# Performance work log

Measured on AMD Instinct MI355X. Metric: run time of the kernel, lower is better.

Reference implementation:

```python
import jax, jax.numpy as jnp
import numpy as np

NUM_HEADS = 8
NUM_GROUPS = 32
EPS = 1e-5


def group_norm(x, gamma, beta):
    # x: (B, C, N)
    B, C, N = x.shape
    xg = x.reshape(B, NUM_GROUPS, (C // NUM_GROUPS) * N)
    mean = xg.mean(axis=-1, keepdims=True)
    var = xg.var(axis=-1, keepdims=True)
    xg = (xg - mean) * jax.lax.rsqrt(var + EPS)
    x = xg.reshape(B, C, N)
    return x * gamma[None, :, None] + beta[None, :, None]


def setup_inputs() -> dict:
    key = jax.random.key(0)
    ks = jax.random.split(key, 7)
    B, C, H, W = 16, 512, 32, 32
    return {
        "x": jax.random.normal(ks[0], (B, C, H, W), dtype=jnp.float32),
        "gamma": jax.random.uniform(ks[1], (C,), dtype=jnp.float32, minval=0.5, maxval=1.5),
        "beta": jax.random.normal(ks[2], (C,), dtype=jnp.float32) * 0.1,
        "w_qkv": jax.random.normal(ks[3], (3 * C, C), dtype=jnp.float32) * 0.02,
        "b_qkv": jax.random.normal(ks[4], (3 * C,), dtype=jnp.float32) * 0.01,
        "w_proj": jax.random.normal(ks[5], (C, C), dtype=jnp.float32) * 0.02,
        "b_proj": jax.random.normal(ks[6], (C,), dtype=jnp.float32) * 0.01,
    }


def reference(x, gamma, beta, w_qkv, b_qkv, w_proj, b_proj):
    B, C, Hs, Ws = x.shape
    N = Hs * Ws
    x3 = x.reshape(B, C, N)
    xn = group_norm(x3, gamma, beta)
    # 1x1 Conv1d == channel-wise linear: (3C, C) x (B, C, N) -> (B, 3C, N)
    qkv = jnp.einsum('oc,bcn->bon', w_qkv, xn) + b_qkv[None, :, None]
    ch = C // NUM_HEADS
    qkv = qkv.reshape(B * NUM_HEADS, 3 * ch, N)
    q, k, v = jnp.split(qkv, 3, axis=1)  # each (B*H, ch, N)
    scale = ch ** (-0.25)
    w = jnp.einsum('bct,bcs->bts', q * scale, k * scale)  # (B*H, N, N)
    w = jax.nn.softmax(w.astype(jnp.float32), axis=-1).astype(q.dtype)
    h = jnp.einsum('bts,bcs->bct', w, v)  # (B*H, ch, N)
    h = h.reshape(B, C, N)
    h = jnp.einsum('oc,bcn->bon', w_proj, h) + b_proj[None, :, None]
    return (x3 + h).reshape(B, C, Hs, Ws)
```

## Files before the change

### kernel.cpp

```cpp
#include <hip/hip_runtime.h>
#include <stdint.h>

typedef unsigned short u16;
typedef float f32x4 __attribute__((ext_vector_type(4)));
typedef short bf16x8 __attribute__((ext_vector_type(8)));

#define DEV __device__ __forceinline__

DEV u16 f2bf(float f) {
  union { float f; unsigned int u; } v; v.f = f;
  unsigned int u = v.u;
  u = (u + 0x7FFFu + ((u >> 16) & 1u)) >> 16;
  return (u16)u;
}

DEV float exp2_(float x) {
#if __has_builtin(__builtin_amdgcn_exp2f)
  return __builtin_amdgcn_exp2f(x);
#else
  return exp2f(x);
#endif
}

DEV unsigned int cvt_pk_bf16(float lo, float hi) {
  unsigned int r;
  asm("v_cvt_pk_bf16_f32 %0, %1, %2" : "=v"(r) : "v"(lo), "v"(hi));
  return r;
}

typedef __attribute__((address_space(1))) const unsigned int* gas_t;
typedef __attribute__((address_space(3))) unsigned int* las_t;
DEV void gload16(const void* g, void* l) {
  __builtin_amdgcn_global_load_lds((gas_t)g, (las_t)l, 16, 0, 0);
}

DEV f32x4 zf4() { f32x4 z = {0.f, 0.f, 0.f, 0.f}; return z; }

static constexpr float QK_SCALE = 0.35355339059327373f;
static constexpr float LOG2E    = 1.4426950408889634f;

static constexpr size_t OFF_WQKV  = 0;
static constexpr size_t OFF_WPROJ = 1572864;
static constexpr size_t OFF_XNT   = 2097152;
static constexpr size_t OFF_Q     = 18874368;
static constexpr size_t OFF_K     = 35651584;
static constexpr size_t OFF_V     = 52428800;
static constexpr size_t OFF_HT    = 69206016;
static constexpr size_t OFF_STATS = 85983232;

__global__ __launch_bounds__(256) void wconv_kernel(const float* __restrict__ wqkv,
                                                    const float* __restrict__ wproj,
                                                    u16* __restrict__ dq, u16* __restrict__ dp) {
  int i = blockIdx.x * 256 + threadIdx.x;
  const float4* src; u16* dst; int j;
  if (i < 196608) { src = (const float4*)wqkv;  dst = dq; j = i; }
  else            { src = (const float4*)wproj; dst = dp; j = i - 196608; }
  float4 v = src[j];
  unsigned int lo = (unsigned int)f2bf(v.x) | ((unsigned int)f2bf(v.y) << 16);
  unsigned int hi = (unsigned int)f2bf(v.z) | ((unsigned int)f2bf(v.w) << 16);
  uint2 o; o.x = lo; o.y = hi;
  *(uint2*)(dst + (size_t)j * 4) = o;
}

__global__ __launch_bounds__(256) void gn_stats_kernel(const float* __restrict__ x,
                                                       float* __restrict__ stats) {
  __shared__ float rs[4], rss[4];
  int grp = blockIdx.x;
  const float4* p = (const float4*)(x + (size_t)grp * 16384);
  float s = 0.f, ss = 0.f;
  for (int i = threadIdx.x; i < 4096; i += 256) {
    float4 v = p[i];
    s  += v.x + v.y + v.z + v.w;
    ss += v.x*v.x + v.y*v.y + v.z*v.z + v.w*v.w;
  }
  #pragma unroll
  for (int off = 32; off > 0; off >>= 1) {
    s  += __shfl_down(s, off);
    ss += __shfl_down(ss, off);
  }
  int wid = threadIdx.x >> 6;
  if ((threadIdx.x & 63) == 0) { rs[wid] = s; rss[wid] = ss; }
  __syncthreads();
  if (threadIdx.x == 0) {
    s  = rs[0] + rs[1] + rs[2] + rs[3];
    ss = rss[0] + rss[1] + rss[2] + rss[3];
    float mean = s * (1.f / 16384.f);
    float var  = ss * (1.f / 16384.f) - mean * mean;
    stats[grp*2 + 0] = mean;
    stats[grp*2 + 1] = rsqrtf(var + 1e-5f);
  }
}

__global__ __launch_bounds__(256) void gn_apply_kernel(const float* __restrict__ x,
                                                       const float* __restrict__ gamma,
                                                       const float* __restrict__ beta,
                                                       const float* __restrict__ stats,
                                                       u16* __restrict__ xnt) {
  __shared__ u16 tile[32 * 520];
  int b = blockIdx.y;
  int n0 = blockIdx.x * 32;
  int tid = threadIdx.x;
  int nseg = tid & 7, crow = tid >> 3;
  for (int it = 0; it < 16; ++it) {
    int c = it * 32 + crow;
    float4 v = *(const float4*)(x + (((size_t)(b*512 + c)) << 10) + n0 + nseg*4);
    int g = c >> 4;
    float mean = stats[(b*32 + g)*2], rstd = stats[(b*32 + g)*2 + 1];
    float ga = gamma[c] * rstd, be = beta[c] - mean * ga;
    int nb = nseg * 4;
    tile[(nb+0)*520 + c] = f2bf(v.x*ga + be);
    tile[(nb+1)*520 + c] = f2bf(v.y*ga + be);
    tile[(nb+2)*520 + c] = f2bf(v.z*ga + be);
    tile[(nb+3)*520 + c] = f2bf(v.w*ga + be);
  }
  __syncthreads();
  int cseg = tid & 63, rw = tid >> 6;
  for (int p = 0; p < 8; ++p) {
    int n = p*4 + rw;
    uint4 v = *(const uint4*)&tile[n*520 + cseg*8];
    *(uint4*)(xnt + ((size_t)(b*1024 + n0 + n))*512 + cseg*8) = v;
  }
}

template<int EPI>
__global__ __launch_bounds__(256) void gemm_kernel(const u16* __restrict__ A,
                                                   const u16* __restrict__ Bm,
                                                   const float* __restrict__ bias,
                                                   u16* __restrict__ Qp, u16* __restrict__ Kp,
                                                   u16* __restrict__ Vp,
                                                   const float* __restrict__ xres,
                                                   float* __restrict__ outp) {
  __shared__ u16 lds[2 * 128 * 64];
  u16* Als = lds;
  u16* Bls = lds + 128 * 64;
  int tid = threadIdx.x, lane = tid & 63, wid = tid >> 6;
  int tl = lane & 15, g = lane >> 4;
  int wm = wid >> 1, wn = wid & 1;
  int tM = blockIdx.y, tN = blockIdx.x;
  int o0 = tM * 128, n0 = tN * 128;
  f32x4 acc[4][4];
  #pragma unroll
  for (int i = 0; i < 4; ++i)
    #pragma unroll
    for (int j = 0; j < 4; ++j) acc[i][j] = zf4();

  int rl = lane >> 3, sg = lane & 7;
  const u16* Ag = A  + (size_t)(o0 + wid*32 + rl) * 512 + ((sg ^ rl) << 3);
  const u16* Bg = Bm + (size_t)(n0 + wid*32 + rl) * 512 + ((sg ^ rl) << 3);
  u16* Alw = Als + wid*32*64;
  u16* Blw = Bls + wid*32*64;

  for (int kt = 0; kt < 8; ++kt) {
    #pragma unroll
    for (int q = 0; q < 4; ++q) {
      gload16(Ag + (size_t)q*8*512 + kt*64, Alw + q*8*64);
      gload16(Bg + (size_t)q*8*512 + kt*64, Blw + q*8*64);
    }
    __syncthreads();
    #pragma unroll
    for (int kk = 0; kk < 2; ++kk) {
      bf16x8 av[4], bv[4];
      #pragma unroll
      for (int mi = 0; mi < 4; ++mi)
        av[mi] = *(const bf16x8*)&Als[(wm*64 + mi*16 + tl)*64 + (((kk*4 + g) ^ (tl & 7)) << 3)];
      #pragma unroll
      for (int ni = 0; ni < 4; ++ni)
        bv[ni] = *(const bf16x8*)&Bls[(wn*64 + ni*16 + tl)*64 + (((kk*4 + g) ^ (tl & 7)) << 3)];
      #pragma unroll
      for (int mi = 0; mi < 4; ++mi)
        #pragma unroll
        for (int ni = 0; ni < 4; ++ni)
          acc[mi][ni] = __builtin_amdgcn_mfma_f32_16x16x32_bf16(av[mi], bv[ni], acc[mi][ni], 0, 0, 0);
    }
    __syncthreads();
  }

  if (EPI == 1) {
    #pragma unroll
    for (int mi = 0; mi < 4; ++mi) {
      int mb = mi*16 + (g << 2);
      float4 bs = *(const float4*)&bias[o0 + wm*64 + mb];
      const float* bsf = (const float*)&bs;
      #pragma unroll
      for (int ni = 0; ni < 4; ++ni) {
        int n_g = n0 + wn*64 + ni*16 + tl;
        int bb = n_g >> 10, n = n_g & 1023;
        #pragma unroll
        for (int rr = 0; rr < 4; ++rr) {
          int o_g = o0 + wm*64 + mb + rr;
          size_t oi = (((size_t)(bb*512 + o_g)) << 10) + n;
          outp[oi] = acc[mi][ni][rr] + bsf[rr] + xres[oi];
        }
      }
    }
    return;
  }

  __syncthreads();
  int a = 2*tM + wm;
  int head = a / 3;
  int sect = a - head*3;
  float sc = (sect == 0) ? QK_SCALE : (sect == 1 ? QK_SCALE * LOG2E : 1.f);
  u16* wl = lds + wid * (64*64);
  #pragma unroll
  for (int mi = 0; mi < 4; ++mi) {
    int mb = mi*16 + (g << 2);
    float4 bs = *(const float4*)&bias[o0 + wm*64 + mb];
    const float* bsf = (const float*)&bs;
    #pragma unroll
    for (int ni = 0; ni < 4; ++ni) {
      int nl = ni*16 + tl;
      #pragma unroll
      for (int rr = 0; rr < 4; ++rr) {
        float val = (acc[mi][ni][rr] + bsf[rr]) * sc;
        int ml = mb + rr;
        if (sect < 2) wl[nl*64 + (ml ^ ((nl & 7) << 3))] = f2bf(val);
        else          wl[ml*64 + (nl ^ ((ml & 7) << 3))] = f2bf(val);
      }
    }
  }
  int n_wb = n0 + wn*64;
  int bb = n_wb >> 10, nn0 = n_wb & 1023;
  int bh = bb*8 + head;
  #pragma unroll
  for (int p = 0; p < 8; ++p) {
    int row = p*8 + (lane >> 3), sgg = lane & 7;
    uint4 v = *(const uint4*)&wl[row*64 + ((sgg ^ (row & 7)) << 3)];
    if (sect == 0)
      *(uint4*)(Qp + (((size_t)bh) << 16) + (size_t)(nn0 + row)*64 + sgg*8) = v;
    else if (sect == 1)
      *(uint4*)(Kp + (((size_t)bh) << 16) + (size_t)(nn0 + row)*64 + sgg*8) = v;
    else
      *(uint4*)(Vp + (((size_t)bh) << 16) + (size_t)row*1024 + nn0 + sgg*8) = v;
  }
}

__global__ __launch_bounds__(256, 4) void attn_kernel(const u16* __restrict__ Qp,
                                                      const u16* __restrict__ Kp,
                                                      const u16* __restrict__ Vp,
                                                      u16* __restrict__ Hp) {
  __shared__ u16 Kls[64 * 64];
  __shared__ u16 Vls[64 * 64];
  __shared__ u16 Pls[4 * 32 * 64];
  int tid = threadIdx.x, lane = tid & 63, w = tid >> 6;
  int id = blockIdx.x;
  int bh = ((id >> 6) << 3) | (id & 7);
  int tblk = (id >> 3) & 7;
  int t0 = tblk * 128 + w * 32;
  size_t hb = ((size_t)bh) << 16;
  int tl = lane & 15, g = lane >> 4;

  bf16x8 bq[2][2];
  #pragma unroll
  for (int tf = 0; tf < 2; ++tf)
    #pragma unroll
    for (int kk = 0; kk < 2; ++kk)
      bq[tf][kk] = *(const bf16x8*)(Qp + hb + (size_t)(t0 + tf*16 + tl)*64 + kk*32 + g*8);

  f32x4 oacc[4][2];
  #pragma unroll
  for (int ci = 0; ci < 4; ++ci)
    #pragma unroll
    for (int tf = 0; tf < 2; ++tf) oacc[ci][tf] = zf4();
  float l_run[2] = {0.f, 0.f};
  u16* pw = Pls + w * (32 * 64);
  int sr = tid >> 3, sseg = tid & 7;
  int xsw = (tl & 7) << 3;

  for (int s0 = 0; s0 < 1024; s0 += 64) {
    #pragma unroll
    for (int p = 0; p < 2; ++p) {
      int row = p*32 + sr;
      int woff = row*64 + ((sseg ^ (row & 7)) << 3);
      *(uint4*)&Kls[woff] = *(const uint4*)(Kp + hb + (size_t)(s0 + row)*64 + sseg*8);
      *(uint4*)&Vls[woff] = *(const uint4*)(Vp + hb + (size_t)row*1024 + s0 + sseg*8);
    }
    __syncthreads();

    f32x4 sfr[2][4];
    #pragma unroll
    for (int tf = 0; tf < 2; ++tf)
      #pragma unroll
      for (int ni = 0; ni < 4; ++ni) sfr[tf][ni] = zf4();
    __builtin_amdgcn_s_setprio(1);
    #pragma unroll
    for (int kk = 0; kk < 2; ++kk) {
      bf16x8 ak[4];
      #pragma unroll
      for (int ni = 0; ni < 4; ++ni)
        ak[ni] = *(const bf16x8*)&Kls[(ni*16 + tl)*64 + ((((kk*4 + g) << 3)) ^ xsw)];
      #pragma unroll
      for (int tf = 0; tf < 2; ++tf)
        #pragma unroll
        for (int ni = 0; ni < 4; ++ni)
          sfr[tf][ni] = __builtin_amdgcn_mfma_f32_16x16x32_bf16(ak[ni], bq[tf][kk], sfr[tf][ni], 0, 0, 0);
    }
    __builtin_amdgcn_s_setprio(0);

    #pragma unroll
    for (int tf = 0; tf < 2; ++tf) {
      int trow = tf*16 + tl;
      int rsw = (trow & 7) << 3;
      float lt = 0.f;
      #pragma unroll
      for (int ni = 0; ni < 4; ++ni) {
        float p0 = exp2_(sfr[tf][ni][0]);
        float p1 = exp2_(sfr[tf][ni][1]);
        float p2 = exp2_(sfr[tf][ni][2]);
        float p3 = exp2_(sfr[tf][ni][3]);
        lt += (p0 + p1) + (p2 + p3);
        uint2 pkv;
        pkv.x = cvt_pk_bf16(p0, p1);
        pkv.y = cvt_pk_bf16(p2, p3);
        *(uint2*)&pw[trow*64 + ((ni*16 + g*4) ^ rsw)] = pkv;
      }
      l_run[tf] += lt;
    }

    __builtin_amdgcn_s_setprio(1);
    #pragma unroll
    for (int kk = 0; kk < 2; ++kk) {
      bf16x8 av[4];
      #pragma unroll
      for (int ci = 0; ci < 4; ++ci)
        av[ci] = *(const bf16x8*)&Vls[(ci*16 + tl)*64 + ((((kk*4 + g) << 3)) ^ xsw)];
      #pragma unroll
      for (int tf = 0; tf < 2; ++tf) {
        int trow = tf*16 + tl;
        bf16x8 bp = *(const bf16x8*)&pw[trow*64 + (((kk*4 + g) << 3) ^ ((trow & 7) << 3))];
        #pragma unroll
        for (int ci = 0; ci < 4; ++ci)
          oacc[ci][tf] = __builtin_amdgcn_mfma_f32_16x16x32_bf16(av[ci], bp, oacc[ci][tf], 0, 0, 0);
      }
    }
    __builtin_amdgcn_s_setprio(0);
    __syncthreads();
  }

  #pragma unroll
  for (int tf = 0; tf < 2; ++tf) {
    float l = l_run[tf];
    l += __shfl_xor(l, 16);
    l += __shfl_xor(l, 32);
    float inv = 1.f / l;
    int trow = tf*16 + tl;
    int rsw = (trow & 7) << 3;
    #pragma unroll
    for (int ci = 0; ci < 4; ++ci) {
      uint2 pkv;
      pkv.x = cvt_pk_bf16(oacc[ci][tf][0]*inv, oacc[ci][tf][1]*inv);
      pkv.y = cvt_pk_bf16(oacc[ci][tf][2]*inv, oacc[ci][tf][3]*inv);
      *(uint2*)&pw[trow*64 + ((ci*16 + g*4) ^ rsw)] = pkv;
    }
  }
  int b = bh >> 3, head = bh & 7;
  #pragma unroll
  for (int p = 0; p < 4; ++p) {
    int row = p*8 + (lane >> 3), sgg = lane & 7;
    uint4 v = *(const uint4*)&pw[row*64 + ((sgg ^ (row & 7)) << 3)];
    *(uint4*)(Hp + ((size_t)(b*1024 + t0 + row))*512 + head*64 + sgg*8) = v;
  }
}

extern "C" void kernel_launch(void* const* d_in, const int* in_sizes, int n_in,
                              void* d_out, int out_size, void* d_ws, size_t ws_size,
                              hipStream_t stream) {
  const float* x     = (const float*)d_in[0];
  const float* gamma = (const float*)d_in[1];
  const float* beta  = (const float*)d_in[2];
  const float* wqkv  = (const float*)d_in[3];
  const float* bqkv  = (const float*)d_in[4];
  const float* wproj = (const float*)d_in[5];
  const float* bproj = (const float*)d_in[6];
  float* out = (float*)d_out;
  char* ws = (char*)d_ws;
  u16* wqkv_bf  = (u16*)(ws + OFF_WQKV);
  u16* wproj_bf = (u16*)(ws + OFF_WPROJ);
  u16* xnt = (u16*)(ws + OFF_XNT);
  u16* Qp  = (u16*)(ws + OFF_Q);
  u16* Kp  = (u16*)(ws + OFF_K);
  u16* Vp  = (u16*)(ws + OFF_V);
  u16* Hp  = (u16*)(ws + OFF_HT);
  float* stats = (float*)(ws + OFF_STATS);

  wconv_kernel<<<1024, 256, 0, stream>>>(wqkv, wproj, wqkv_bf, wproj_bf);
  gn_stats_kernel<<<512, 256, 0, stream>>>(x, stats);
  gn_apply_kernel<<<dim3(32, 16), 256, 0, stream>>>(x, gamma, beta, stats, xnt);
  gemm_kernel<0><<<dim3(128, 12), 256, 0, stream>>>(wqkv_bf, xnt, bqkv, Qp, Kp, Vp, nullptr, nullptr);
  attn_kernel<<<1024, 256, 0, stream>>>(Qp, Kp, Vp, Hp);
  gemm_kernel<1><<<dim3(128, 4), 256, 0, stream>>>(wproj_bf, Hp, bproj, nullptr, nullptr, nullptr, x, out);
}
```

Measured before the change: 204.5 us.

## Fuse group-norm stats and apply into one kernel; double-buffer GEMM LDS tiles

Merges the group-norm statistics and apply kernels into a single kernel per (batch, group). Each block keeps its 16 channels x 1024 positions in registers, reduces them, normalizes, transposes through LDS and writes the bf16 transposed activations. This avoids reading x twice and saves a launch. The GEMM kernel now double-buffers its A/B LDS tiles, prefetching the next k-tile while computing the current one, which doubles LDS use per block and adds register pressure.

```diff
diff --git a/kernel.cpp b/kernel.cpp
--- a/kernel.cpp
+++ b/kernel.cpp
@@ -46,7 +46,6 @@
 static constexpr size_t OFF_K     = 35651584;
 static constexpr size_t OFF_V     = 52428800;
 static constexpr size_t OFF_HT    = 69206016;
-static constexpr size_t OFF_STATS = 85983232;
 
 __global__ __launch_bounds__(256) void wconv_kernel(const float* __restrict__ wqkv,
                                                     const float* __restrict__ wproj,
@@ -62,63 +61,59 @@
   *(uint2*)(dst + (size_t)j * 4) = o;
 }
 
-__global__ __launch_bounds__(256) void gn_stats_kernel(const float* __restrict__ x,
-                                                       float* __restrict__ stats) {
-  __shared__ float rs[4], rss[4];
+__global__ __launch_bounds__(256, 4) void gn_fused_kernel(const float* __restrict__ x,
+                                                          const float* __restrict__ gamma,
+                                                          const float* __restrict__ beta,
+                                                          u16* __restrict__ xnt) {
+  __shared__ u16 Tls[16 * 1024];
+  __shared__ float rs[4], rss[4], bcast[2];
   int grp = blockIdx.x;
+  int b = grp >> 5, g = grp & 31;
+  int tid = threadIdx.x;
   const float4* p = (const float4*)(x + (size_t)grp * 16384);
+  float4 v[16];
   float s = 0.f, ss = 0.f;
-  for (int i = threadIdx.x; i < 4096; i += 256) {
-    float4 v = p[i];
-    s  += v.x + v.y + v.z + v.w;
-    ss += v.x*v.x + v.y*v.y + v.z*v.z + v.w*v.w;
+  #pragma unroll
+  for (int it = 0; it < 16; ++it) {
+    v[it] = p[it * 256 + tid];
+    s  += v[it].x + v[it].y + v[it].z + v[it].w;
+    ss += v[it].x*v[it].x + v[it].y*v[it].y + v[it].z*v[it].z + v[it].w*v[it].w;
   }
   #pragma unroll
   for (int off = 32; off > 0; off >>= 1) {
     s  += __shfl_down(s, off);
     ss += __shfl_down(ss, off);
   }
-  int wid = threadIdx.x >> 6;
-  if ((threadIdx.x & 63) == 0) { rs[wid] = s; rss[wid] = ss; }
+  int wid = tid >> 6;
+  if ((tid & 63) == 0) { rs[wid] = s; rss[wid] = ss; }
   __syncthreads();
-  if (threadIdx.x == 0) {
+  if (tid == 0) {
     s  = rs[0] + rs[1] + rs[2] + rs[3];
     ss = rss[0] + rss[1] + rss[2] + rss[3];
     float mean = s * (1.f / 16384.f);
     float var  = ss * (1.f / 16384.f) - mean * mean;
-    stats[grp*2 + 0] = mean;
-    stats[grp*2 + 1] = rsqrtf(var + 1e-5f);
-  }
-}
-
-__global__ __launch_bounds__(256) void gn_apply_kernel(const float* __restrict__ x,
-                                                       const float* __restrict__ gamma,
-                                                       const float* __restrict__ beta,
-                                                       const float* __restrict__ stats,
-                                                       u16* __restrict__ xnt) {
-  __shared__ u16 tile[32 * 520];
-  int b = blockIdx.y;
-  int n0 = blockIdx.x * 32;
-  int tid = threadIdx.x;
-  int nseg = tid & 7, crow = tid >> 3;
+    bcast[0] = mean;
+    bcast[1] = rsqrtf(var + 1e-5f);
+  }
+  __syncthreads();
+  float mean = bcast[0], rstd = bcast[1];
+  #pragma unroll
   for (int it = 0; it < 16; ++it) {
-    int c = it * 32 + crow;
-    float4 v = *(const float4*)(x + (((size_t)(b*512 + c)) << 10) + n0 + nseg*4);
-    int g = c >> 4;
-    float mean = stats[(b*32 + g)*2], rstd = stats[(b*32 + g)*2 + 1];
+    int c = g*16 + it;
     float ga = gamma[c] * rstd, be = beta[c] - mean * ga;
-    int nb = nseg * 4;
-    tile[(nb+0)*520 + c] = f2bf(v.x*ga + be);
-    tile[(nb+1)*520 + c] = f2bf(v.y*ga + be);
-    tile[(nb+2)*520 + c] = f2bf(v.z*ga + be);
-    tile[(nb+3)*520 + c] = f2bf(v.w*ga + be);
+    uint2 pk;
+    pk.x = cvt_pk_bf16(v[it].x*ga + be, v[it].y*ga + be);
+    pk.y = cvt_pk_bf16(v[it].z*ga + be, v[it].w*ga + be);
+    *(uint2*)&Tls[it*1024 + tid*4] = pk;
   }
   __syncthreads();
-  int cseg = tid & 63, rw = tid >> 6;
-  for (int p = 0; p < 8; ++p) {
-    int n = p*4 + rw;
-    uint4 v = *(const uint4*)&tile[n*520 + cseg*8];
-    *(uint4*)(xnt + ((size_t)(b*1024 + n0 + n))*512 + cseg*8) = v;
+  u16* dst = xnt + ((size_t)b * 1024) * 512 + g*16;
+  for (int r = 0; r < 8; ++r) {
+    int idx = r*256 + tid, n = idx >> 1, half = idx & 1;
+    u16 tmp[8];
+    #pragma unroll
+    for (int cc = 0; cc < 8; ++cc) tmp[cc] = Tls[(half*8 + cc)*1024 + n];
+    *(uint4*)(dst + (size_t)n*512 + half*8) = *(uint4*)tmp;
   }
 }
 
@@ -130,9 +125,7 @@
                                                    u16* __restrict__ Vp,
                                                    const float* __restrict__ xres,
                                                    float* __restrict__ outp) {
-  __shared__ u16 lds[2 * 128 * 64];
-  u16* Als = lds;
-  u16* Bls = lds + 128 * 64;
+  __shared__ u16 lds[4 * 128 * 64];
   int tid = threadIdx.x, lane = tid & 63, wid = tid >> 6;
   int tl = lane & 15, g = lane >> 4;
   int wm = wid >> 1, wn = wid & 1;
@@ -147,16 +140,26 @@
   int rl = lane >> 3, sg = lane & 7;
   const u16* Ag = A  + (size_t)(o0 + wid*32 + rl) * 512 + ((sg ^ rl) << 3);
   const u16* Bg = Bm + (size_t)(n0 + wid*32 + rl) * 512 + ((sg ^ rl) << 3);
-  u16* Alw = Als + wid*32*64;
-  u16* Blw = Bls + wid*32*64;
-
+  int wofs = wid*32*64;
+
+#define STAGE_GEMM(buf, kt)                                                     \
+  {                                                                             \
+    u16* Ad = lds + (buf)*16384 + wofs;                                         \
+    u16* Bd = lds + (buf)*16384 + 8192 + wofs;                                  \
+    _Pragma("unroll")                                                           \
+    for (int q = 0; q < 4; ++q) {                                               \
+      gload16(Ag + (size_t)q*8*512 + (kt)*64, Ad + q*8*64);                     \
+      gload16(Bg + (size_t)q*8*512 + (kt)*64, Bd + q*8*64);                     \
+    }                                                                           \
+  }
+
+  STAGE_GEMM(0, 0);
+  __syncthreads();
   for (int kt = 0; kt < 8; ++kt) {
-    #pragma unroll
-    for (int q = 0; q < 4; ++q) {
-      gload16(Ag + (size_t)q*8*512 + kt*64, Alw + q*8*64);
-      gload16(Bg + (size_t)q*8*512 + kt*64, Blw + q*8*64);
-    }
-    __syncthreads();
+    int cur = kt & 1;
+    if (kt < 7) STAGE_GEMM(cur ^ 1, kt + 1);
+    const u16* Als = lds + cur*16384;
+    const u16* Bls = lds + cur*16384 + 8192;
     #pragma unroll
     for (int kk = 0; kk < 2; ++kk) {
       bf16x8 av[4], bv[4];
@@ -174,6 +177,7 @@
     }
     __syncthreads();
   }
+#undef STAGE_GEMM
 
   if (EPI == 1) {
     #pragma unroll
@@ -196,7 +200,6 @@
     return;
   }
 
-  __syncthreads();
   int a = 2*tM + wm;
   int head = a / 3;
   int sect = a - head*3;
@@ -381,11 +384,9 @@
   u16* Kp  = (u16*)(ws + OFF_K);
   u16* Vp  = (u16*)(ws + OFF_V);
   u16* Hp  = (u16*)(ws + OFF_HT);
-  float* stats = (float*)(ws + OFF_STATS);
 
   wconv_kernel<<<1024, 256, 0, stream>>>(wqkv, wproj, wqkv_bf, wproj_bf);
-  gn_stats_kernel<<<512, 256, 0, stream>>>(x, stats);
-  gn_apply_kernel<<<dim3(32, 16), 256, 0, stream>>>(x, gamma, beta, stats, xnt);
+  gn_fused_kernel<<<512, 256, 0, stream>>>(x, gamma, beta, xnt);
   gemm_kernel<0><<<dim3(128, 12), 256, 0, stream>>>(wqkv_bf, xnt, bqkv, Qp, Kp, Vp, nullptr, nullptr);
   attn_kernel<<<1024, 256, 0, stream>>>(Qp, Kp, Vp, Hp);
   gemm_kernel<1><<<dim3(128, 4), 256, 0, stream>>>(wproj_bf, Hp, bproj, nullptr, nullptr, nullptr, x, out);
```

New measurement: 194.5 us. 4.9% less time.
